# Optimization experiments

Measured on AMD Instinct MI355X. Metric: run time of the kernel, lower is better.

Reference implementation:

```python
import jax, jax.numpy as jnp
import numpy as np

D = 14          # AOI image size (pixels per side)
K, B, F = 2, 512, 512   # spots, AOI batch, frame batch
N_T, N_F = 512, 1024    # total targets, total frames in target_locs table


def setup_inputs() -> dict:
    key = jax.random.key(0)
    ks = jax.random.split(key, 8)
    height = jax.random.uniform(ks[0], (K, B, F), dtype=jnp.float32) * 3000.0
    width = jax.random.uniform(ks[1], (K, B, F), dtype=jnp.float32) + 1.0  # keep > 0
    x = jax.random.normal(ks[2], (K, B, F), dtype=jnp.float32)
    y = jax.random.normal(ks[3], (K, B, F), dtype=jnp.float32)
    background = jax.random.uniform(ks[4], (B, F), dtype=jnp.float32) * 100.0
    target_locs = jax.random.normal(ks[5], (N_T, N_F, 2), dtype=jnp.float32) + (D - 1) / 2.0
    n_idx = jax.random.randint(ks[6], (B, 1), 0, N_T)
    f = jax.random.randint(ks[7], (F,), 0, N_F)
    return {"height": height, "width": width, "x": x, "y": y,
            "background": background, "target_locs": target_locs,
            "n_idx": n_idx, "f": f}


def reference(height, width, x, y, background, target_locs, n_idx, f):
    # spot centers: target_locs[n_idx, f] broadcasts [B,1] x [F] -> [B,F,2]
    locs = target_locs[n_idx, f]                 # [B, F, 2]
    sx = locs[..., 0] + x                        # [K, B, F] (i-coordinate)
    sy = locs[..., 1] + y                        # [K, B, F] (j-coordinate)
    pix = jnp.arange(D, dtype=height.dtype)      # [D]
    # separable squared distances (avoids a [K,B,F,D,D,2] intermediate)
    dx2 = (pix - sx[..., None]) ** 2             # [K, B, F, D]
    dy2 = (pix - sy[..., None]) ** 2             # [K, B, F, D]
    w2 = width * width                           # [K, B, F]
    # isotropic MVN density: exp(-r^2/(2 w^2)) / (2*pi*w^2)
    logp = (-jnp.log(2.0 * jnp.pi * w2)[..., None, None]
            - (dx2[..., :, None] + dy2[..., None, :]) / (2.0 * w2)[..., None, None])
    gaussian_spot = jnp.exp(logp)                # [K, B, F, D, D]
    img = (height[..., None, None] * gaussian_spot).sum(axis=0, keepdims=True)  # [1,B,F,D,D]
    return img + background[None, ..., None, None]
```

## Files before the change

### kernel.cpp

```cpp
#include <hip/hip_runtime.h>
#include <math.h>


#define DD 14
#define BB 512
#define FFRAMES 512
#define NF_TAB 1024
#define PAIRS_PER_BLOCK 64
#define BLOCK 256

__global__ __launch_bounds__(BLOCK) void gauss_spot_kernel(
    const float* __restrict__ height, const float* __restrict__ width,
    const float* __restrict__ xoff, const float* __restrict__ yoff,
    const float* __restrict__ background, const float* __restrict__ target_locs,
    const int* __restrict__ n_idx, const int* __restrict__ f_tab,
    float* __restrict__ out)
{
    __shared__ float lds[PAIRS_PER_BLOCK][4][DD];
    __shared__ float bg_s[PAIRS_PER_BLOCK];

    const int tid = threadIdx.x;
    const int pair_local = tid >> 2;
    const int sel = tid & 3;
    const int k = sel >> 1;
    const int isY = sel & 1;
    const int pair = blockIdx.x * PAIRS_PER_BLOCK + pair_local;
    const int b = pair >> 9;
    const int fi = pair & (FFRAMES - 1);

    const int n = n_idx[b];
    const int ff = f_tab[fi];
    const float loc = target_locs[(n * NF_TAB + ff) * 2 + isY];
    const int idx = k * (BB * FFRAMES) + pair;
    const float w = width[idx];
    const float off = isY ? yoff[idx] : xoff[idx];
    const float s = loc + off;
    const float inv2w2 = 1.0f / (2.0f * w * w);
    const float coef = isY ? 1.0f : height[idx] * inv2w2 * 0.31830988618379067f;
    const float a = inv2w2 * 1.4426950408889634f;

    #pragma unroll
    for (int i = 0; i < DD; ++i) {
        float d = (float)i - s;
        lds[pair_local][sel][i] = coef * exp2f(-d * d * a);
    }
    if (sel == 0) bg_s[pair_local] = background[pair];
    __syncthreads();

    float4* outv = (float4*)(out + (size_t)blockIdx.x * (PAIRS_PER_BLOCK * DD * DD));
    const int NV = PAIRS_PER_BLOCK * DD * DD / 4;
    for (int v = tid; v < NV; v += BLOCK) {
        int p = v / 49;
        int pix0 = (v - p * 49) * 4;
        float bg = bg_s[p];
        float4 r;
        #pragma unroll
        for (int e = 0; e < 4; ++e) {
            int pix = pix0 + e;
            int i = pix / DD;
            int j = pix - i * DD;
            ((float*)&r)[e] = bg
                + lds[p][0][i] * lds[p][1][j]
                + lds[p][2][i] * lds[p][3][j];
        }
        outv[v] = r;
    }
}

extern "C" void kernel_launch(void* const* d_in, const int* in_sizes, int n_in,
                              void* d_out, int out_size, void* d_ws, size_t ws_size,
                              hipStream_t stream) {
    const float* height      = (const float*)d_in[0];
    const float* width       = (const float*)d_in[1];
    const float* x           = (const float*)d_in[2];
    const float* y           = (const float*)d_in[3];
    const float* background  = (const float*)d_in[4];
    const float* target_locs = (const float*)d_in[5];
    const int*   n_idx       = (const int*)d_in[6];
    const int*   f           = (const int*)d_in[7];
    float* out = (float*)d_out;

    const int total_pairs = BB * FFRAMES;
    const int grid = total_pairs / PAIRS_PER_BLOCK;
    gauss_spot_kernel<<<grid, BLOCK, 0, stream>>>(
        height, width, x, y, background, target_locs, n_idx, f, out);
}
```

Measured before the change: 221.5 us.

## Interleave spot factors in LDS, vectorize reads, use nontemporal stores

Changes the shared-memory layout to interleaved float2 rows (k=0,1 side by side) padded to 18 entries, so each output float4 needs a few vector LDS loads instead of sixteen scalar ones. Replaces the per-element divisions with a multiply-shift and an incrementally updated (pair, remainder) counter, and uses fused multiply-adds. Output is written with nontemporal stores to avoid polluting the cache with the large streaming image. The wrap logic assumes four pixels never span more than one row boundary, which holds for a 14-pixel row with even offsets.

```diff
diff --git a/kernel.cpp b/kernel.cpp
--- a/kernel.cpp
+++ b/kernel.cpp
@@ -8,6 +8,9 @@
 #define NF_TAB 1024
 #define PAIRS_PER_BLOCK 64
 #define BLOCK 256
+#define LROW 18
+
+typedef float nat_f4 __attribute__((ext_vector_type(4)));
 
 __global__ __launch_bounds__(BLOCK) void gauss_spot_kernel(
     const float* __restrict__ height, const float* __restrict__ width,
@@ -16,15 +19,16 @@
     const int* __restrict__ n_idx, const int* __restrict__ f_tab,
     float* __restrict__ out)
 {
-    __shared__ float lds[PAIRS_PER_BLOCK][4][DD];
+    __shared__ __align__(16) float2 LX[PAIRS_PER_BLOCK][LROW];
+    __shared__ __align__(16) float2 LY[PAIRS_PER_BLOCK][LROW];
     __shared__ float bg_s[PAIRS_PER_BLOCK];
 
     const int tid = threadIdx.x;
-    const int pair_local = tid >> 2;
+    const int pl = tid >> 2;
     const int sel = tid & 3;
     const int k = sel >> 1;
     const int isY = sel & 1;
-    const int pair = blockIdx.x * PAIRS_PER_BLOCK + pair_local;
+    const int pair = blockIdx.x * PAIRS_PER_BLOCK + pl;
     const int b = pair >> 9;
     const int fi = pair & (FFRAMES - 1);
 
@@ -39,31 +43,41 @@
     const float coef = isY ? 1.0f : height[idx] * inv2w2 * 0.31830988618379067f;
     const float a = inv2w2 * 1.4426950408889634f;
 
+    float* dst = isY ? (float*)(&LY[pl][0]) : (float*)(&LX[pl][0]);
     #pragma unroll
     for (int i = 0; i < DD; ++i) {
         float d = (float)i - s;
-        lds[pair_local][sel][i] = coef * exp2f(-d * d * a);
+        dst[2 * i + k] = coef * exp2f(-d * d * a);
     }
-    if (sel == 0) bg_s[pair_local] = background[pair];
+    if (sel == 0) bg_s[pl] = background[pair];
     __syncthreads();
 
-    float4* outv = (float4*)(out + (size_t)blockIdx.x * (PAIRS_PER_BLOCK * DD * DD));
+    nat_f4* outv = (nat_f4*)(out + (size_t)blockIdx.x * (PAIRS_PER_BLOCK * DD * DD));
     const int NV = PAIRS_PER_BLOCK * DD * DD / 4;
+    int p = tid / 49;
+    int rem = tid - p * 49;
     for (int v = tid; v < NV; v += BLOCK) {
-        int p = v / 49;
-        int pix0 = (v - p * 49) * 4;
-        float bg = bg_s[p];
-        float4 r;
-        #pragma unroll
-        for (int e = 0; e < 4; ++e) {
-            int pix = pix0 + e;
-            int i = pix / DD;
-            int j = pix - i * DD;
-            ((float*)&r)[e] = bg
-                + lds[p][0][i] * lds[p][1][j]
-                + lds[p][2][i] * lds[p][3][j];
-        }
-        outv[v] = r;
+        const int pix0 = rem * 4;
+        const int i0 = (pix0 * 2341) >> 15;
+        const int j0 = pix0 - i0 * DD;
+        const bool wrap = (j0 == 12);
+        const int jb = wrap ? 0 : (j0 + 2);
+
+        const float2 xa  = LX[p][i0];
+        const float2 x23 = LX[p][i0 + (wrap ? 1 : 0)];
+        const float4 ya  = *(const float4*)(&LY[p][j0]);
+        const float4 yb  = *(const float4*)(&LY[p][jb]);
+        const float bg = bg_s[p];
+
+        nat_f4 r;
+        r.x = fmaf(xa.y,  ya.y, fmaf(xa.x,  ya.x, bg));
+        r.y = fmaf(xa.y,  ya.w, fmaf(xa.x,  ya.z, bg));
+        r.z = fmaf(x23.y, yb.y, fmaf(x23.x, yb.x, bg));
+        r.w = fmaf(x23.y, yb.w, fmaf(x23.x, yb.z, bg));
+        __builtin_nontemporal_store(r, &outv[v]);
+
+        rem += 11; p += 5;
+        if (rem >= 49) { rem -= 49; p += 1; }
     }
 }
 
```

After: 232.3 us. +4.9%, slower.
